# Optimization experiments

Hardware: AMD Instinct MI355X
Metric: run time of the kernel (lower is better)

## Reference

```python
import jax, jax.numpy as jnp
import numpy as np

N, E = 50000, 800000          # n_nodes, n_edges
IN_C, OUT_C = 128, 64         # in_channels, out_channels


def setup_inputs() -> dict:
    key = jax.random.key(0)
    ks = jax.random.split(key, 12)
    def w(k, i, o):
        return jax.random.normal(k, (i, o), jnp.float32) / np.float32(np.sqrt(i))
    return {
        "x": jax.random.normal(ks[0], (N, IN_C), jnp.float32),
        "edge_index": jax.random.randint(ks[1], (2, E), 0, N),
        "eps": jax.random.normal(ks[2], (N, OUT_C), jnp.float32),
        # encoder GCNConv1: in -> 2*out
        "W_e1": w(ks[3], IN_C, 2 * OUT_C), "b_e1": jnp.zeros((2 * OUT_C,), jnp.float32),
        # encoder GCNConv2: 2*out -> out
        "W_e2": w(ks[4], 2 * OUT_C, OUT_C), "b_e2": jnp.zeros((OUT_C,), jnp.float32),
        # fc_mu / fc_logvar: out -> out
        "W_mu": w(ks[5], OUT_C, OUT_C), "b_mu": jnp.zeros((OUT_C,), jnp.float32),
        "W_lv": w(ks[6], OUT_C, OUT_C), "b_lv": jnp.zeros((OUT_C,), jnp.float32),
        # decoder GCNConv1: out -> in
        "W_d1": w(ks[7], OUT_C, IN_C), "b_d1": jnp.zeros((IN_C,), jnp.float32),
        # decoder GCNConv2: in -> in
        "W_d2": w(ks[8], IN_C, IN_C), "b_d2": jnp.zeros((IN_C,), jnp.float32),
    }


def _gcn_norm(edge_index, n):
    # PyG gcn_norm: add self-loops, symmetric D^-1/2 A D^-1/2 normalization
    loop = jnp.arange(n)
    src = jnp.concatenate([edge_index[0], loop])
    dst = jnp.concatenate([edge_index[1], loop])
    deg = jax.ops.segment_sum(jnp.ones_like(dst, jnp.float32), dst, num_segments=n)
    dinv = jnp.where(deg > 0, deg ** -0.5, 0.0)
    norm = dinv[src] * dinv[dst]  # [E + N]
    return src, dst, norm


def _gcn_conv(x, W, b, src, dst, norm, n):
    h = x @ W                       # linear transform first (small channel dim)
    msg = h[src] * norm[:, None]    # gather + edge scaling
    return jax.ops.segment_sum(msg, dst, num_segments=n) + b  # scatter-add + bias


def reference(x, edge_index, eps, W_e1, b_e1, W_e2, b_e2, W_mu, b_mu, W_lv, b_lv, W_d1, b_d1, W_d2, b_d2):
    n = x.shape[0]
    src, dst, norm = _gcn_norm(edge_index, n)
    # encoder
    h = jax.nn.relu(_gcn_conv(x, W_e1, b_e1, src, dst, norm, n))
    h = _gcn_conv(h, W_e2, b_e2, src, dst, norm, n)
    mu = h @ W_mu + b_mu
    logvar = h @ W_lv + b_lv
    # reparameterize (training mode)
    z = mu + eps * jnp.exp(0.5 * logvar)
    # decoder
    d = jax.nn.relu(_gcn_conv(z, W_d1, b_d1, src, dst, norm, n))
    d = _gcn_conv(d, W_d2, b_d2, src, dst, norm, n)
    return (d, mu, logvar)
```

## Files before the change

### kernel.cpp

```cpp
#include <hip/hip_runtime.h>
#include <math.h>

typedef unsigned short u16;
typedef unsigned int u32;
typedef __attribute__((ext_vector_type(8))) short s16x8;
typedef __attribute__((ext_vector_type(4))) float f32x4;

__device__ __forceinline__ float bf2f(u16 u) { return __uint_as_float(((u32)u) << 16); }
__device__ __forceinline__ u16 f2bf(float f) {
    u32 u = __float_as_uint(f);
    return (u16)((u + 0x7fffu + ((u >> 16) & 1u)) >> 16);
}

union U4 { u32 u[4]; s16x8 v; };

__device__ __forceinline__ s16x8 pack_hi(f32x4 x0, f32x4 x1) {
    U4 r;
    r.u[0] = (__float_as_uint(x0.y) & 0xFFFF0000u) | (__float_as_uint(x0.x) >> 16);
    r.u[1] = (__float_as_uint(x0.w) & 0xFFFF0000u) | (__float_as_uint(x0.z) >> 16);
    r.u[2] = (__float_as_uint(x1.y) & 0xFFFF0000u) | (__float_as_uint(x1.x) >> 16);
    r.u[3] = (__float_as_uint(x1.w) & 0xFFFF0000u) | (__float_as_uint(x1.z) >> 16);
    return r.v;
}
__device__ __forceinline__ s16x8 pack_lo(f32x4 x0, f32x4 x1) {
    float e0 = x0.x - __uint_as_float(__float_as_uint(x0.x) & 0xFFFF0000u);
    float e1 = x0.y - __uint_as_float(__float_as_uint(x0.y) & 0xFFFF0000u);
    float e2 = x0.z - __uint_as_float(__float_as_uint(x0.z) & 0xFFFF0000u);
    float e3 = x0.w - __uint_as_float(__float_as_uint(x0.w) & 0xFFFF0000u);
    float e4 = x1.x - __uint_as_float(__float_as_uint(x1.x) & 0xFFFF0000u);
    float e5 = x1.y - __uint_as_float(__float_as_uint(x1.y) & 0xFFFF0000u);
    float e6 = x1.z - __uint_as_float(__float_as_uint(x1.z) & 0xFFFF0000u);
    float e7 = x1.w - __uint_as_float(__float_as_uint(x1.w) & 0xFFFF0000u);
    U4 r;
    r.u[0] = (__float_as_uint(e1) & 0xFFFF0000u) | (__float_as_uint(e0) >> 16);
    r.u[1] = (__float_as_uint(e3) & 0xFFFF0000u) | (__float_as_uint(e2) >> 16);
    r.u[2] = (__float_as_uint(e5) & 0xFFFF0000u) | (__float_as_uint(e4) >> 16);
    r.u[3] = (__float_as_uint(e7) & 0xFFFF0000u) | (__float_as_uint(e6) >> 16);
    return r.v;
}

#define BSHIFT 9
#define BSIZE 512
#define BCAP 10240

struct PackArgs { const float* w[6]; };


__device__ __forceinline__ void pack_body(const PackArgs& pa, u16* __restrict__ out, int g, int t) {
    const int Ks[6] = {128, 128, 64, 64, 64, 128};
    const int Ms[6] = {128, 64, 64, 64, 128, 128};
    const int Off[6] = {0, 16384, 24576, 28672, 32768, 40960};
    int s = g >> 6;
    int id = (g & 63) * 256 + t;
    int K = Ks[s], M = Ms[s];
    if (id >= K * M) return;
    int ms = (M == 128) ? 7 : 6;
    int k = id >> ms, c = id & (M - 1);
    int chunk = k >> 5, j = k & 7, lq = (k >> 3) & 3;
    int ct = c >> 4, ln = (c & 15) + (lq << 4);
    out[Off[s] + (chunk * (M >> 4) + ct) * 512 + ln * 8 + j] = f2bf(pa.w[s][id]);
}


__global__ __launch_bounds__(256) void k_bin_pack(const int* __restrict__ ei, int E, int NB, int C,
                                                  int* __restrict__ bin_cursor, u32* __restrict__ binned,
                                                  PackArgs pa, u16* __restrict__ wpk) {
    __shared__ int sh[256];
    const int t = threadIdx.x;
    if ((int)blockIdx.x >= C) {
        pack_body(pa, wpk, blockIdx.x - C, t);
        return;
    }
    int* hist = sh;
    int* base_l = sh + 128;
    const int e0 = blockIdx.x * 4096;
    int sreg[16], dreg[16];
#pragma unroll
    for (int j = 0; j < 16; ++j) {
        int e = e0 + j * 256 + t;
        if (e < E) {
            sreg[j] = ei[e];
            dreg[j] = ei[E + e];
        } else {
            dreg[j] = -1;
        }
    }
    if (t < NB) hist[t] = 0;
    __syncthreads();
#pragma unroll
    for (int j = 0; j < 16; ++j)
        if (dreg[j] >= 0) atomicAdd(&hist[dreg[j] >> BSHIFT], 1);
    __syncthreads();
    if (t < NB) {
        base_l[t] = atomicAdd(&bin_cursor[t], hist[t]);
        hist[t] = 0;
    }
    __syncthreads();
#pragma unroll
    for (int j = 0; j < 16; ++j)
        if (dreg[j] >= 0) {
            int b = dreg[j] >> BSHIFT;
            int pos = base_l[b] + atomicAdd(&hist[b], 1);
            if (pos < BCAP) binned[(size_t)b * BCAP + pos] = ((u32)(dreg[j] & (BSIZE - 1)) << 17) | (u32)sreg[j];
        }
}


template <int K, int M, int RT, int NSET, bool XBF16, bool OUT_BF16, bool BREL>
__device__ __forceinline__ void gemm_tile(const void* __restrict__ Xv, const u16* __restrict__ Bpk,
                                          const float* __restrict__ b0, const float* __restrict__ b1,
                                          const float* __restrict__ eps,
                                          void* __restrict__ Y0, float* __restrict__ Y1,
                                          u16* __restrict__ Z, int N, int col0, int row0, int t) {
    constexpr int CH = K / 32;
    constexpr int TPM = M >> 4;
    constexpr int SETSTRIDE = CH * TPM * 512;
    const int lane = t & 63, w = t >> 6;
    const int l15 = lane & 15, q = lane >> 4;

    s16x8 Bfr[NSET * CH * 4];
#pragma unroll
    for (int s = 0; s < NSET; ++s)
#pragma unroll
        for (int ch = 0; ch < CH; ++ch)
#pragma unroll
            for (int ct = 0; ct < 4; ++ct)
                Bfr[(s * CH + ch) * 4 + ct] =
                    *(const s16x8*)&Bpk[(size_t)s * SETSTRIDE + ((ch * TPM) + (col0 >> 4) + ct) * 512 + lane * 8];

    f32x4 acc[NSET][RT][4];
#pragma unroll
    for (int s = 0; s < NSET; ++s)
#pragma unroll
        for (int rt = 0; rt < RT; ++rt)
#pragma unroll
            for (int ct = 0; ct < 4; ++ct) acc[s][rt][ct] = 0.f;

#pragma unroll
    for (int ch = 0; ch < CH; ++ch) {
#pragma unroll
        for (int rt = 0; rt < RT; ++rt) {
            int r = row0 + (w * RT + rt) * 16 + l15;
            r = r < N ? r : N - 1;
            s16x8 ah, al;
            if (XBF16) {
                ah = *(const s16x8*)((const u16*)Xv + (size_t)r * K + (ch << 5) + (q << 3));
            } else {
                const float* xp = (const float*)Xv + (size_t)r * K + (ch << 5) + (q << 3);
                f32x4 x0 = *(const f32x4*)xp;
                f32x4 x1 = *(const f32x4*)(xp + 4);
                ah = pack_hi(x0, x1);
                al = pack_lo(x0, x1);
            }
#pragma unroll
            for (int s = 0; s < NSET; ++s)
#pragma unroll
                for (int ct = 0; ct < 4; ++ct) {
                    int fb = (s * CH + ch) * 4 + ct;
                    acc[s][rt][ct] = __builtin_amdgcn_mfma_f32_16x16x32_bf16(ah, Bfr[fb], acc[s][rt][ct], 0, 0, 0);
                    if (!XBF16)
                        acc[s][rt][ct] = __builtin_amdgcn_mfma_f32_16x16x32_bf16(al, Bfr[fb], acc[s][rt][ct], 0, 0, 0);
                }
        }
    }

#pragma unroll
    for (int rt = 0; rt < RT; ++rt)
#pragma unroll
        for (int ct = 0; ct < 4; ++ct)
#pragma unroll
            for (int reg = 0; reg < 4; ++reg) {
                int row = row0 + (w * RT + rt) * 16 + q * 4 + reg;
                if (row >= N) continue;
                int col = col0 + ct * 16 + l15;
                float v = acc[0][rt][ct][reg];
                if (BREL) v = fmaxf(v + b0[col], 0.f);
                if (OUT_BF16)
                    ((u16*)Y0)[(size_t)row * M + col] = f2bf(v);
                else
                    ((float*)Y0)[(size_t)row * M + col] = v;
            }
}


__global__ __launch_bounds__(256, 3) void k_cnt_gemm1(const u32* __restrict__ binned,
                                                      const int* __restrict__ bin_cursor, int N, int NB,
                                                      int* __restrict__ cnt, float* __restrict__ dinv,
                                                      int* __restrict__ row_start, int* __restrict__ cursor,
                                                      const float* __restrict__ x, const u16* __restrict__ wpk,
                                                      u16* __restrict__ R1) {
    __shared__ int cnt_l[BSIZE];
    __shared__ int wave_sum[5];
    __shared__ int base_s;
    const int t = threadIdx.x;
    const int b = blockIdx.x;
    if (b >= NB) {
        gemm_tile<128, 128, 2, 1, false, true, false>(x, wpk, nullptr, nullptr, nullptr, R1, nullptr, nullptr,
                                                      N, 0, (b - NB) * 128, t);
        return;
    }
    const int lane = t & 63, w = t >> 6;
    cnt_l[t] = 0;
    cnt_l[t + 256] = 0;
    __syncthreads();
    const int n = min(bin_cursor[b], BCAP);
    for (int i = t; i < n; i += 256) atomicAdd(&cnt_l[binned[(size_t)b * BCAP + i] >> 17], 1);
    __syncthreads();
    int c0 = cnt_l[2 * t], c1 = cnt_l[2 * t + 1];
    int p0 = (c0 + 7) & ~7, p1 = (c1 + 7) & ~7;
    int s = p0 + p1;
    int incl = s;
#pragma unroll
    for (int o = 1; o < 64; o <<= 1) {
        int v = __shfl_up(incl, o, 64);
        if (lane >= o) incl += v;
    }
    if (lane == 63) wave_sum[w] = incl;
    __syncthreads();
    if (t == 0) {
        int acc = 0;
#pragma unroll
        for (int i = 0; i < 4; ++i) {
            int v = wave_sum[i];
            wave_sum[i] = acc;
            acc += v;
        }
        base_s = atomicAdd(cursor, acc);
    }
    __syncthreads();
    int excl = incl - s + wave_sum[w] + base_s;
    int v0 = b * BSIZE + 2 * t;
    if (v0 < N) {
        cnt[v0] = c0;
        dinv[v0] = rsqrtf((float)(c0 + 1));
        row_start[v0] = excl;
    }
    if (v0 + 1 < N) {
        cnt[v0 + 1] = c1;
        dinv[v0 + 1] = rsqrtf((float)(c1 + 1));
        row_start[v0 + 1] = excl + p0;
    }
}


__global__ __launch_bounds__(256, 3) void k_scat_gemm1(const u32* __restrict__ binned,
                                                       const int* __restrict__ bin_cursor,
                                                       const int* __restrict__ row_start,
                                                       const float* __restrict__ dinv, int N, int NB,
                                                       int2* __restrict__ edges,
                                                       const float* __restrict__ x, const u16* __restrict__ wpk,
                                                       u16* __restrict__ R1) {
    __shared__ float dv_l[BSIZE];
    __shared__ int rs_l[BSIZE];
    __shared__ int fill_l[BSIZE];
    const int t = threadIdx.x;
    const int b = blockIdx.x;
    if (b >= NB) {
        gemm_tile<128, 128, 2, 1, false, true, false>(x, wpk, nullptr, nullptr, nullptr, R1, nullptr, nullptr,
                                                      N, 64, (b - NB) * 128, t);
        return;
    }
#pragma unroll
    for (int hh = 0; hh < 2; ++hh) {
        int d = t + hh * 256;
        int v = b * BSIZE + d;
        bool ok = v < N;
        dv_l[d] = ok ? dinv[v] : 0.f;
        rs_l[d] = ok ? row_start[v] : 0;
        fill_l[d] = 0;
    }
    __syncthreads();
    const int n = min(bin_cursor[b], BCAP);
    for (int i = t; i < n; i += 256) {
        u32 e = binned[(size_t)b * BCAP + i];
        int dl = e >> 17;
        int src = e & 0x1FFFF;
        float wgt = dinv[src] * dv_l[dl];
        int pos = rs_l[dl] + atomicAdd(&fill_l[dl], 1);
        edges[pos] = make_int2(src, __float_as_int(wgt));
    }
    __syncthreads();
#pragma unroll
    for (int hh = 0; hh < 2; ++hh) {
        int d = t + hh * 256;
        int v = b * BSIZE + d;
        if (v >= N) continue;
        int c = fill_l[d];
        int pc = (c + 7) & ~7;
        for (int j = c; j < pc; ++j) edges[rs_l[d] + j] = make_int2(0, 0);
    }
}


__device__ __forceinline__ void agg_row128(const u32* __restrict__ hp, const int2* __restrict__ edges,
                                           int start, int pc, int lane, float& a0, float& a1) {
    if (!pc) return;
    int2 e[8];
#pragma unroll
    for (int j = 0; j < 8; ++j) e[j] = edges[start + j];
    for (int i = 0; i < pc; i += 8) {
        u32 h[8];
        float wv[8];
#pragma unroll
        for (int j = 0; j < 8; ++j) {
            h[j] = hp[(size_t)e[j].x * 64 + lane];
            wv[j] = __int_as_float(e[j].y);
        }
        if (i + 8 < pc) {
#pragma unroll
            for (int j = 0; j < 8; ++j) e[j] = edges[start + i + 8 + j];
        }
#pragma unroll
        for (int j = 0; j < 8; ++j) {
            a0 = fmaf(wv[j], bf2f((u16)h[j]), a0);
            a1 = fmaf(wv[j], bf2f((u16)(h[j] >> 16)), a1);
        }
    }
}

__device__ __forceinline__ void agg_row64(const u16* __restrict__ hin, const int2* __restrict__ edges,
                                          int start, int pc, int lane, float& a0) {
    if (!pc) return;
    int2 e[8];
#pragma unroll
    for (int j = 0; j < 8; ++j) e[j] = edges[start + j];
    for (int i = 0; i < pc; i += 8) {
        u16 h[8];
        float wv[8];
#pragma unroll
        for (int j = 0; j < 8; ++j) {
            h[j] = hin[(size_t)e[j].x * 64 + lane];
            wv[j] = __int_as_float(e[j].y);
        }
        if (i + 8 < pc) {
#pragma unroll
            for (int j = 0; j < 8; ++j) e[j] = edges[start + i + 8 + j];
        }
#pragma unroll
        for (int j = 0; j < 8; ++j) a0 = fmaf(wv[j], bf2f(h[j]), a0);
    }
}


__global__ __launch_bounds__(256) void k_agg1_g2(const u16* __restrict__ R1, const int2* __restrict__ edges,
                                                 const int* __restrict__ row_start, const int* __restrict__ cnt,
                                                 const float* __restrict__ dinv, const float* __restrict__ be1,
                                                 const u16* __restrict__ Bpk, u16* __restrict__ W1, int N) {
    __shared__ u16 Ar[16 * 136];
    const int t = threadIdx.x, w = t >> 6, lane = t & 63;
    const u32* hp = (const u32*)R1;
#pragma unroll
    for (int i = 0; i < 4; ++i) {
        const int r = w * 4 + i;
        const int v = blockIdx.x * 16 + r;
        float a0 = 0.f, a1 = 0.f;
        if (v < N) {
            const int start = __builtin_amdgcn_readfirstlane(row_start[v]);
            const int c = __builtin_amdgcn_readfirstlane(cnt[v]);
            const int pc = (c + 7) & ~7;
            agg_row128(hp, edges, start, pc, lane, a0, a1);
            float dv = dinv[v], sw = dv * dv;
            u32 hs = hp[(size_t)v * 64 + lane];
            a0 = fmaf(sw, bf2f((u16)hs), a0);
            a1 = fmaf(sw, bf2f((u16)(hs >> 16)), a1);
            float2 bp = ((const float2*)be1)[lane];
            a0 += bp.x;
            a1 += bp.y;
            a0 = fmaxf(a0, 0.f);
            a1 = fmaxf(a1, 0.f);
        }
        ((u32*)Ar)[r * 68 + lane] = (u32)f2bf(a0) | ((u32)f2bf(a1) << 16);
    }
    __syncthreads();
    const int l15 = lane & 15, q = lane >> 4;
    f32x4 acc = 0.f;
#pragma unroll
    for (int ch = 0; ch < 4; ++ch) {
        s16x8 ah = *(const s16x8*)&Ar[l15 * 136 + ch * 32 + q * 8];
        s16x8 b = *(const s16x8*)&Bpk[(ch * 4 + w) * 512 + lane * 8];
        acc = __builtin_amdgcn_mfma_f32_16x16x32_bf16(ah, b, acc, 0, 0, 0);
    }
#pragma unroll
    for (int reg = 0; reg < 4; ++reg) {
        int row = blockIdx.x * 16 + q * 4 + reg;
        if (row >= N) continue;
        int col = w * 16 + l15;
        W1[(size_t)row * 64 + col] = f2bf(acc[reg]);
    }
}


__global__ __launch_bounds__(256) void k_agg2_mlv(const u16* __restrict__ W1, const int2* __restrict__ edges,
                                                  const int* __restrict__ row_start, const int* __restrict__ cnt,
                                                  const float* __restrict__ dinv, const float* __restrict__ be2,
                                                  const u16* __restrict__ Bmu, const u16* __restrict__ Blv,
                                                  const float* __restrict__ bmu, const float* __restrict__ blv,
                                                  const float* __restrict__ eps,
                                                  float* __restrict__ out_mu, float* __restrict__ out_lv,
                                                  u16* __restrict__ Zb, int N) {
    __shared__ float Af[16 * 68];
    const int t = threadIdx.x, w = t >> 6, lane = t & 63;
#pragma unroll
    for (int i = 0; i < 4; ++i) {
        const int r = w * 4 + i;
        const int v = blockIdx.x * 16 + r;
        float a0 = 0.f;
        if (v < N) {
            const int start = __builtin_amdgcn_readfirstlane(row_start[v]);
            const int c = __builtin_amdgcn_readfirstlane(cnt[v]);
            const int pc = (c + 7) & ~7;
            agg_row64(W1, edges, start, pc, lane, a0);
            float dv = dinv[v];
            a0 = fmaf(dv * dv, bf2f(W1[(size_t)v * 64 + lane]), a0);
            a0 += be2[lane];
        }
        Af[r * 68 + lane] = a0;
    }
    __syncthreads();
    const int l15 = lane & 15, q = lane >> 4;
    f32x4 accm = 0.f, accl = 0.f;
#pragma unroll
    for (int ch = 0; ch < 2; ++ch) {
        f32x4 x0 = *(const f32x4*)&Af[l15 * 68 + ch * 32 + q * 8];
        f32x4 x1 = *(const f32x4*)&Af[l15 * 68 + ch * 32 + q * 8 + 4];
        s16x8 ah = pack_hi(x0, x1);
        s16x8 al = pack_lo(x0, x1);
        s16x8 bm = *(const s16x8*)&Bmu[(ch * 4 + w) * 512 + lane * 8];
        s16x8 bl = *(const s16x8*)&Blv[(ch * 4 + w) * 512 + lane * 8];
        accm = __builtin_amdgcn_mfma_f32_16x16x32_bf16(ah, bm, accm, 0, 0, 0);
        accm = __builtin_amdgcn_mfma_f32_16x16x32_bf16(al, bm, accm, 0, 0, 0);
        accl = __builtin_amdgcn_mfma_f32_16x16x32_bf16(ah, bl, accl, 0, 0, 0);
        accl = __builtin_amdgcn_mfma_f32_16x16x32_bf16(al, bl, accl, 0, 0, 0);
    }
#pragma unroll
    for (int reg = 0; reg < 4; ++reg) {
        int row = blockIdx.x * 16 + q * 4 + reg;
        if (row >= N) continue;
        int col = w * 16 + l15;
        size_t o = (size_t)row * 64 + col;
        float mu = accm[reg] + bmu[col];
        float lv = accl[reg] + blv[col];
        out_mu[o] = mu;
        out_lv[o] = lv;
        Zb[o] = f2bf(mu + eps[o] * expf(0.5f * lv));
    }
}


__global__ __launch_bounds__(256) void k_agg3_d12(const u16* __restrict__ Zb, const int2* __restrict__ edges,
                                                  const int* __restrict__ row_start, const int* __restrict__ cnt,
                                                  const float* __restrict__ dinv,
                                                  const u16* __restrict__ Bd1, const u16* __restrict__ Bd2,
                                                  const float* __restrict__ bd1, u16* __restrict__ R1, int N) {
    __shared__ float Zr[16 * 68];
    __shared__ u16 Br[16 * 136];
    const int t = threadIdx.x, w = t >> 6, lane = t & 63;
#pragma unroll
    for (int i = 0; i < 4; ++i) {
        const int r = w * 4 + i;
        const int v = blockIdx.x * 16 + r;
        float a0 = 0.f;
        if (v < N) {
            const int start = __builtin_amdgcn_readfirstlane(row_start[v]);
            const int c = __builtin_amdgcn_readfirstlane(cnt[v]);
            const int pc = (c + 7) & ~7;
            agg_row64(Zb, edges, start, pc, lane, a0);
            float dv = dinv[v];
            a0 = fmaf(dv * dv, bf2f(Zb[(size_t)v * 64 + lane]), a0);
        }
        Zr[r * 68 + lane] = a0;
    }
    __syncthreads();
    const int l15 = lane & 15, q = lane >> 4;
    {
        f32x4 acc1[2];
        acc1[0] = 0.f;
        acc1[1] = 0.f;
#pragma unroll
        for (int ch = 0; ch < 2; ++ch) {
            f32x4 x0 = *(const f32x4*)&Zr[l15 * 68 + ch * 32 + q * 8];
            f32x4 x1 = *(const f32x4*)&Zr[l15 * 68 + ch * 32 + q * 8 + 4];
            s16x8 ah = pack_hi(x0, x1);
            s16x8 al = pack_lo(x0, x1);
#pragma unroll
            for (int cti = 0; cti < 2; ++cti) {
                s16x8 b = *(const s16x8*)&Bd1[(ch * 8 + w + cti * 4) * 512 + lane * 8];
                acc1[cti] = __builtin_amdgcn_mfma_f32_16x16x32_bf16(ah, b, acc1[cti], 0, 0, 0);
                acc1[cti] = __builtin_amdgcn_mfma_f32_16x16x32_bf16(al, b, acc1[cti], 0, 0, 0);
            }
        }
#pragma unroll
        for (int cti = 0; cti < 2; ++cti)
#pragma unroll
            for (int reg = 0; reg < 4; ++reg) {
                int col = (w + cti * 4) * 16 + l15;
                float v = fmaxf(acc1[cti][reg] + bd1[col], 0.f);
                Br[(q * 4 + reg) * 136 + col] = f2bf(v);
            }
    }
    __syncthreads();
    {
        f32x4 acc2[2];
        acc2[0] = 0.f;
        acc2[1] = 0.f;
#pragma unroll
        for (int ch = 0; ch < 4; ++ch) {
            s16x8 ah = *(const s16x8*)&Br[l15 * 136 + ch * 32 + q * 8];
#pragma unroll
            for (int cti = 0; cti < 2; ++cti) {
                s16x8 b = *(const s16x8*)&Bd2[(ch * 8 + w + cti * 4) * 512 + lane * 8];
                acc2[cti] = __builtin_amdgcn_mfma_f32_16x16x32_bf16(ah, b, acc2[cti], 0, 0, 0);
            }
        }
#pragma unroll
        for (int cti = 0; cti < 2; ++cti)
#pragma unroll
            for (int reg = 0; reg < 4; ++reg) {
                int row = blockIdx.x * 16 + q * 4 + reg;
                if (row >= N) continue;
                int col = (w + cti * 4) * 16 + l15;
                R1[(size_t)row * 128 + col] = f2bf(acc2[cti][reg]);
            }
    }
}


__global__ __launch_bounds__(256) void k_agg4(const u16* __restrict__ hin, const int2* __restrict__ edges,
                                              const int* __restrict__ row_start, const int* __restrict__ cnt,
                                              const float* __restrict__ dinv, const float* __restrict__ bias,
                                              float* __restrict__ out, int N) {
    const int v = blockIdx.x * 4 + (threadIdx.x >> 6);
    const int lane = threadIdx.x & 63;
    if (v >= N) return;
    const int start = __builtin_amdgcn_readfirstlane(row_start[v]);
    const int c = __builtin_amdgcn_readfirstlane(cnt[v]);
    const int pc = (c + 7) & ~7;
    const u32* hp = (const u32*)hin;
    float a0 = 0.f, a1 = 0.f;
    agg_row128(hp, edges, start, pc, lane, a0, a1);
    float dv = dinv[v], sw = dv * dv;
    u32 hs = hp[(size_t)v * 64 + lane];
    a0 = fmaf(sw, bf2f((u16)hs), a0);
    a1 = fmaf(sw, bf2f((u16)(hs >> 16)), a1);
    float2 bp = ((const float2*)bias)[lane];
    a0 += bp.x;
    a1 += bp.y;
    ((float2*)out)[(size_t)v * 64 + lane] = make_float2(a0, a1);
}


extern "C" void kernel_launch(void* const* d_in, const int* in_sizes, int n_in,
                              void* d_out, int out_size, void* d_ws, size_t ws_size,
                              hipStream_t stream) {
    const float* x = (const float*)d_in[0];
    const int* ei = (const int*)d_in[1];
    const float* eps = (const float*)d_in[2];
    const float* We1 = (const float*)d_in[3];
    const float* be1 = (const float*)d_in[4];
    const float* We2 = (const float*)d_in[5];
    const float* be2 = (const float*)d_in[6];
    const float* Wmu = (const float*)d_in[7];
    const float* bmu = (const float*)d_in[8];
    const float* Wlv = (const float*)d_in[9];
    const float* blv = (const float*)d_in[10];
    const float* Wd1 = (const float*)d_in[11];
    const float* bd1 = (const float*)d_in[12];
    const float* Wd2 = (const float*)d_in[13];
    const float* bd2 = (const float*)d_in[14];

    const int N = in_sizes[0] / 128;
    const int E = in_sizes[1] / 2;
    const int ECAP = E + 8 * N;
    const int NB = (N + BSIZE - 1) >> BSHIFT;
    const int C = (E + 4095) / 4096;

    int* bin_cursor = (int*)d_ws;
    int* cursor = bin_cursor + 128;
    float* dinv = (float*)(bin_cursor + 256);
    int* row_start = (int*)(dinv + N);
    int* cnt = row_start + N;
    int2* edges = (int2*)(cnt + N);
    u16* R1 = (u16*)(edges + ECAP);
    u16* W1 = R1 + (size_t)N * 128;
    u16* Zb = W1 + (size_t)N * 128;
    u16* Wpk = Zb + (size_t)N * 128;
    u32* binned = (u32*)W1;

    float* out_d = (float*)d_out;
    float* out_mu = out_d + (size_t)N * 128;
    float* out_lv = out_mu + (size_t)N * 64;

    hipMemsetAsync(d_ws, 0, 256 * 4, stream);

    PackArgs pa;
    pa.w[0] = We1; pa.w[1] = We2; pa.w[2] = Wmu; pa.w[3] = Wlv; pa.w[4] = Wd1; pa.w[5] = Wd2;

    const int RB128 = (N + 127) / 128;
    const int AB = (N + 3) / 4;
    const int FB = (N + 15) / 16;

    k_bin_pack<<<dim3(C + 384), dim3(256), 0, stream>>>(ei, E, NB, C, bin_cursor, binned, pa, Wpk);
    k_cnt_gemm1<<<dim3(NB + RB128), dim3(256), 0, stream>>>(binned, bin_cursor, N, NB, cnt, dinv, row_start,
                                                            cursor, x, Wpk, R1);
    k_scat_gemm1<<<dim3(NB + RB128), dim3(256), 0, stream>>>(binned, bin_cursor, row_start, dinv, N, NB,
                                                             edges, x, Wpk, R1);
    k_agg1_g2<<<dim3(FB), dim3(256), 0, stream>>>(R1, edges, row_start, cnt, dinv, be1, Wpk + 16384, W1, N);
    k_agg2_mlv<<<dim3(FB), dim3(256), 0, stream>>>(W1, edges, row_start, cnt, dinv, be2, Wpk + 24576,
                                                   Wpk + 28672, bmu, blv, eps, out_mu, out_lv, Zb, N);
    k_agg3_d12<<<dim3(FB), dim3(256), 0, stream>>>(Zb, edges, row_start, cnt, dinv, Wpk + 32768,
                                                   Wpk + 40960, bd1, R1, N);
    k_agg4<<<dim3(AB), dim3(256), 0, stream>>>(R1, edges, row_start, cnt, dinv, bd2, out_d, N);
}
```

Measured before the change: 299.8 us.

## Merge count and scatter kernels, defer source weight, XCD-sliced persistent final aggregation

The degree-count and edge-scatter kernels become one, since each block owns its destination bin. The stored edge weight is now only dinv[dst], and dinv[src] is multiplied in during every aggregation, which drops the cross-block dependency on dinv before scatter. The final aggregation turns into a persistent kernel that reads the hardware XCD id and gives each XCD a 16-column channel slice, pulled through per-slice atomic chunk counters. This is meant to improve L2 locality of gathers per XCD, and it uses nontemporal stores. The cost is an extra dinv gather per edge in all four aggregations, plus a dependence on the assumption that blocks are spread evenly across XCDs (xcd&3 covers only 4 slices).

Result: slower. 403.6 us (+34.6%).

```diff
diff --git a/kernel.cpp b/kernel.cpp
--- a/kernel.cpp
+++ b/kernel.cpp
@@ -5,6 +5,7 @@
 typedef unsigned int u32;
 typedef __attribute__((ext_vector_type(8))) short s16x8;
 typedef __attribute__((ext_vector_type(4))) float f32x4;
+typedef __attribute__((ext_vector_type(2))) float f32x2;
 
 __device__ __forceinline__ float bf2f(u16 u) { return __uint_as_float(((u32)u) << 16); }
 __device__ __forceinline__ u16 f2bf(float f) {
@@ -183,20 +184,25 @@
 }
 
 
-__global__ __launch_bounds__(256, 3) void k_cnt_gemm1(const u32* __restrict__ binned,
-                                                      const int* __restrict__ bin_cursor, int N, int NB,
-                                                      int* __restrict__ cnt, float* __restrict__ dinv,
-                                                      int* __restrict__ row_start, int* __restrict__ cursor,
-                                                      const float* __restrict__ x, const u16* __restrict__ wpk,
-                                                      u16* __restrict__ R1) {
+__global__ __launch_bounds__(256, 3) void k_graph_gemm1(const u32* __restrict__ binned,
+                                                        const int* __restrict__ bin_cursor, int N, int NB,
+                                                        int* __restrict__ cnt, float* __restrict__ dinv,
+                                                        int* __restrict__ row_start, int* __restrict__ cursor,
+                                                        int2* __restrict__ edges,
+                                                        const float* __restrict__ x, const u16* __restrict__ wpk,
+                                                        u16* __restrict__ R1) {
     __shared__ int cnt_l[BSIZE];
+    __shared__ int rs_l[BSIZE];
+    __shared__ float dv_l[BSIZE];
+    __shared__ int fill_l[BSIZE];
     __shared__ int wave_sum[5];
     __shared__ int base_s;
     const int t = threadIdx.x;
     const int b = blockIdx.x;
     if (b >= NB) {
+        int idx = b - NB;
         gemm_tile<128, 128, 2, 1, false, true, false>(x, wpk, nullptr, nullptr, nullptr, R1, nullptr, nullptr,
-                                                      N, 0, (b - NB) * 128, t);
+                                                      N, (idx & 1) * 64, (idx >> 1) * 128, t);
         return;
     }
     const int lane = t & 63, w = t >> 6;
@@ -229,55 +235,31 @@
     }
     __syncthreads();
     int excl = incl - s + wave_sum[w] + base_s;
+    float d0 = rsqrtf((float)(c0 + 1)), d1 = rsqrtf((float)(c1 + 1));
     int v0 = b * BSIZE + 2 * t;
     if (v0 < N) {
         cnt[v0] = c0;
-        dinv[v0] = rsqrtf((float)(c0 + 1));
+        dinv[v0] = d0;
         row_start[v0] = excl;
     }
     if (v0 + 1 < N) {
         cnt[v0 + 1] = c1;
-        dinv[v0 + 1] = rsqrtf((float)(c1 + 1));
+        dinv[v0 + 1] = d1;
         row_start[v0 + 1] = excl + p0;
     }
-}
-
-
-__global__ __launch_bounds__(256, 3) void k_scat_gemm1(const u32* __restrict__ binned,
-                                                       const int* __restrict__ bin_cursor,
-                                                       const int* __restrict__ row_start,
-                                                       const float* __restrict__ dinv, int N, int NB,
-                                                       int2* __restrict__ edges,
-                                                       const float* __restrict__ x, const u16* __restrict__ wpk,
-                                                       u16* __restrict__ R1) {
-    __shared__ float dv_l[BSIZE];
-    __shared__ int rs_l[BSIZE];
-    __shared__ int fill_l[BSIZE];
-    const int t = threadIdx.x;
-    const int b = blockIdx.x;
-    if (b >= NB) {
-        gemm_tile<128, 128, 2, 1, false, true, false>(x, wpk, nullptr, nullptr, nullptr, R1, nullptr, nullptr,
-                                                      N, 64, (b - NB) * 128, t);
-        return;
-    }
-#pragma unroll
-    for (int hh = 0; hh < 2; ++hh) {
-        int d = t + hh * 256;
-        int v = b * BSIZE + d;
-        bool ok = v < N;
-        dv_l[d] = ok ? dinv[v] : 0.f;
-        rs_l[d] = ok ? row_start[v] : 0;
-        fill_l[d] = 0;
-    }
-    __syncthreads();
-    const int n = min(bin_cursor[b], BCAP);
+    rs_l[2 * t] = excl;
+    rs_l[2 * t + 1] = excl + p0;
+    dv_l[2 * t] = d0;
+    dv_l[2 * t + 1] = d1;
+    fill_l[2 * t] = 0;
+    fill_l[2 * t + 1] = 0;
+    __syncthreads();
     for (int i = t; i < n; i += 256) {
         u32 e = binned[(size_t)b * BCAP + i];
         int dl = e >> 17;
         int src = e & 0x1FFFF;
-        float wgt = dinv[src] * dv_l[dl];
         int pos = rs_l[dl] + atomicAdd(&fill_l[dl], 1);
-        edges[pos] = make_int2(src, __float_as_int(wgt));
+        edges[pos] = make_int2(src, __float_as_int(dv_l[dl]));
     }
     __syncthreads();
 #pragma unroll
@@ -293,6 +275,7 @@
 
 
 __device__ __forceinline__ void agg_row128(const u32* __restrict__ hp, const int2* __restrict__ edges,
+                                           const float* __restrict__ dvg,
                                            int start, int pc, int lane, float& a0, float& a1) {
     if (!pc) return;
     int2 e[8];
@@ -304,7 +287,7 @@
 #pragma unroll
         for (int j = 0; j < 8; ++j) {
             h[j] = hp[(size_t)e[j].x * 64 + lane];
-            wv[j] = __int_as_float(e[j].y);
+            wv[j] = __int_as_float(e[j].y) * dvg[e[j].x];
         }
         if (i + 8 < pc) {
 #pragma unroll
@@ -319,6 +302,7 @@
 }
 
 __device__ __forceinline__ void agg_row64(const u16* __restrict__ hin, const int2* __restrict__ edges,
+                                          const float* __restrict__ dvg,
                                           int start, int pc, int lane, float& a0) {
     if (!pc) return;
     int2 e[8];
@@ -330,7 +314,7 @@
 #pragma unroll
         for (int j = 0; j < 8; ++j) {
             h[j] = hin[(size_t)e[j].x * 64 + lane];
-            wv[j] = __int_as_float(e[j].y);
+            wv[j] = __int_as_float(e[j].y) * dvg[e[j].x];
         }
         if (i + 8 < pc) {
 #pragma unroll
@@ -358,7 +342,7 @@
             const int start = __builtin_amdgcn_readfirstlane(row_start[v]);
             const int c = __builtin_amdgcn_readfirstlane(cnt[v]);
             const int pc = (c + 7) & ~7;
-            agg_row128(hp, edges, start, pc, lane, a0, a1);
+            agg_row128(hp, edges, dinv, start, pc, lane, a0, a1);
             float dv = dinv[v], sw = dv * dv;
             u32 hs = hp[(size_t)v * 64 + lane];
             a0 = fmaf(sw, bf2f((u16)hs), a0);
@@ -409,7 +393,7 @@
             const int start = __builtin_amdgcn_readfirstlane(row_start[v]);
             const int c = __builtin_amdgcn_readfirstlane(cnt[v]);
             const int pc = (c + 7) & ~7;
-            agg_row64(W1, edges, start, pc, lane, a0);
+            agg_row64(W1, edges, dinv, start, pc, lane, a0);
             float dv = dinv[v];
             a0 = fmaf(dv * dv, bf2f(W1[(size_t)v * 64 + lane]), a0);
             a0 += be2[lane];
@@ -464,7 +448,7 @@
             const int start = __builtin_amdgcn_readfirstlane(row_start[v]);
             const int c = __builtin_amdgcn_readfirstlane(cnt[v]);
             const int pc = (c + 7) & ~7;
-            agg_row64(Zb, edges, start, pc, lane, a0);
+            agg_row64(Zb, edges, dinv, start, pc, lane, a0);
             float dv = dinv[v];
             a0 = fmaf(dv * dv, bf2f(Zb[(size_t)v * 64 + lane]), a0);
         }
@@ -525,27 +509,62 @@
 }
 
 
-__global__ __launch_bounds__(256) void k_agg4(const u16* __restrict__ hin, const int2* __restrict__ edges,
-                                              const int* __restrict__ row_start, const int* __restrict__ cnt,
-                                              const float* __restrict__ dinv, const float* __restrict__ bias,
-                                              float* __restrict__ out, int N) {
-    const int v = blockIdx.x * 4 + (threadIdx.x >> 6);
-    const int lane = threadIdx.x & 63;
-    if (v >= N) return;
-    const int start = __builtin_amdgcn_readfirstlane(row_start[v]);
-    const int c = __builtin_amdgcn_readfirstlane(cnt[v]);
-    const int pc = (c + 7) & ~7;
+__global__ __launch_bounds__(256) void k_agg4s(const u16* __restrict__ hin, const int2* __restrict__ edges,
+                                               const int* __restrict__ row_start, const int* __restrict__ cnt,
+                                               const float* __restrict__ dinv, const float* __restrict__ bias,
+                                               float* __restrict__ out, int N, int* __restrict__ cur) {
+    __shared__ int s_c;
+    const int t = threadIdx.x;
+    const int w = t >> 6, l = t & 63;
+    const int sub = l >> 4, li = l & 15;
+    int xcd;
+    asm("s_getreg_b32 %0, hwreg(HW_REG_XCC_ID, 0, 32)" : "=s"(xcd));
+    const int slice = xcd & 3;
+    const int off = slice * 16 + li;
     const u32* hp = (const u32*)hin;
-    float a0 = 0.f, a1 = 0.f;
-    agg_row128(hp, edges, start, pc, lane, a0, a1);
-    float dv = dinv[v], sw = dv * dv;
-    u32 hs = hp[(size_t)v * 64 + lane];
-    a0 = fmaf(sw, bf2f((u16)hs), a0);
-    a1 = fmaf(sw, bf2f((u16)(hs >> 16)), a1);
-    float2 bp = ((const float2*)bias)[lane];
-    a0 += bp.x;
-    a1 += bp.y;
-    ((float2*)out)[(size_t)v * 64 + lane] = make_float2(a0, a1);
+    const int NCH = (N + 511) >> 9;
+    for (;;) {
+        if (t == 0) s_c = atomicAdd(cur + slice, 1);
+        __syncthreads();
+        const int c = s_c;
+        __syncthreads();
+        if (c >= NCH) break;
+        for (int it = 0; it < 32; ++it) {
+            const int v = c * 512 + it * 16 + w * 4 + sub;
+            if (v >= N) continue;
+            const int start = row_start[v];
+            const int pc = (cnt[v] + 7) & ~7;
+            float a0 = 0.f, a1 = 0.f;
+            for (int i = 0; i < pc; i += 8) {
+                int2 e[8];
+#pragma unroll
+                for (int j = 0; j < 8; ++j) e[j] = edges[start + i + j];
+                u32 h[8];
+                float wv[8];
+#pragma unroll
+                for (int j = 0; j < 8; ++j) {
+                    h[j] = hp[(size_t)(u32)e[j].x * 64 + off];
+                    wv[j] = __int_as_float(e[j].y) * dinv[e[j].x];
+                }
+#pragma unroll
+                for (int j = 0; j < 8; ++j) {
+                    a0 = fmaf(wv[j], bf2f((u16)h[j]), a0);
+                    a1 = fmaf(wv[j], bf2f((u16)(h[j] >> 16)), a1);
+                }
+            }
+            float dv = dinv[v], sw = dv * dv;
+            u32 hs = hp[(size_t)v * 64 + off];
+            a0 = fmaf(sw, bf2f((u16)hs), a0);
+            a1 = fmaf(sw, bf2f((u16)(hs >> 16)), a1);
+            float2 bp = ((const float2*)bias)[off];
+            a0 += bp.x;
+            a1 += bp.y;
+            f32x2 o;
+            o.x = a0;
+            o.y = a1;
+            __builtin_nontemporal_store(o, (f32x2*)out + (size_t)v * 64 + off);
+        }
+    }
 }
 
 
@@ -576,6 +595,7 @@
 
     int* bin_cursor = (int*)d_ws;
     int* cursor = bin_cursor + 128;
+    int* slice_cur = bin_cursor + 160;
     float* dinv = (float*)(bin_cursor + 256);
     int* row_start = (int*)(dinv + N);
     int* cnt = row_start + N;
@@ -590,24 +610,21 @@
     float* out_mu = out_d + (size_t)N * 128;
     float* out_lv = out_mu + (size_t)N * 64;
 
-    hipMemsetAsync(d_ws, 0, 256 * 4, stream);
+    hipMemsetAsync(d_ws, 0, 1024, stream);
 
     PackArgs pa;
     pa.w[0] = We1; pa.w[1] = We2; pa.w[2] = Wmu; pa.w[3] = Wlv; pa.w[4] = Wd1; pa.w[5] = Wd2;
 
     const int RB128 = (N + 127) / 128;
-    const int AB = (N + 3) / 4;
     const int FB = (N + 15) / 16;
 
     k_bin_pack<<<dim3(C + 384), dim3(256), 0, stream>>>(ei, E, NB, C, bin_cursor, binned, pa, Wpk);
-    k_cnt_gemm1<<<dim3(NB + RB128), dim3(256), 0, stream>>>(binned, bin_cursor, N, NB, cnt, dinv, row_start,
-                                                            cursor, x, Wpk, R1);
-    k_scat_gemm1<<<dim3(NB + RB128), dim3(256), 0, stream>>>(binned, bin_cursor, row_start, dinv, N, NB,
-                                                             edges, x, Wpk, R1);
+    k_graph_gemm1<<<dim3(NB + 2 * RB128), dim3(256), 0, stream>>>(binned, bin_cursor, N, NB, cnt, dinv,
+                                                                  row_start, cursor, edges, x, Wpk, R1);
     k_agg1_g2<<<dim3(FB), dim3(256), 0, stream>>>(R1, edges, row_start, cnt, dinv, be1, Wpk + 16384, W1, N);
     k_agg2_mlv<<<dim3(FB), dim3(256), 0, stream>>>(W1, edges, row_start, cnt, dinv, be2, Wpk + 24576,
                                                    Wpk + 28672, bmu, blv, eps, out_mu, out_lv, Zb, N);
     k_agg3_d12<<<dim3(FB), dim3(256), 0, stream>>>(Zb, edges, row_start, cnt, dinv, Wpk + 32768,
                                                    Wpk + 40960, bd1, R1, N);
-    k_agg4<<<dim3(AB), dim3(256), 0, stream>>>(R1, edges, row_start, cnt, dinv, bd2, out_d, N);
-}
+    k_agg4s<<<dim3(1024), dim3(256), 0, stream>>>(R1, edges, row_start, cnt, dinv, bd2, out_d, N, slice_cur);
+}
```
